# Optimization experiments

Hardware: AMD Instinct MI355X
Metric: run time of the kernel (lower is better)

Reference implementation:

```python
import jax, jax.numpy as jnp
import numpy as np

K = 3
CHUNK = 1000  # query chunk size for KNN distance tiles
EPS = 1e-8
GRID = 256.0  # coordinate extent (coords / stride in the original)


def _knn3(queries, refs):
    """Brute-force KNN (K=3, squared L2) computed in chunks to bound memory.
    queries: [Q,3], refs: [M,3] -> (dist [Q,3], idx [Q,3] int32)."""
    ref_sq = jnp.sum(refs * refs, axis=-1)  # [M]

    def chunk_fn(q):  # q: [CHUNK,3]
        d = jnp.sum(q * q, -1)[:, None] - 2.0 * (q @ refs.T) + ref_sq[None, :]
        d = jnp.maximum(d, 0.0)  # guard tiny negatives from cancellation
        neg_d, idx = jax.lax.top_k(-d, K)
        return -neg_d, idx

    Q = queries.shape[0]
    qs = queries.reshape(Q // CHUNK, CHUNK, 3)
    dists, idxs = jax.lax.map(chunk_fn, qs)
    return dists.reshape(Q, K), idxs.reshape(Q, K)


def setup_inputs() -> dict:
    key = jax.random.key(0)
    k1, k2, k3, k4 = jax.random.split(key, 4)
    N1, N2, C = 20000, 20000, 8
    xyz1 = jax.random.uniform(k1, (N1, 3), dtype=jnp.float32) * GRID
    point1 = jax.random.normal(k2, (N1, C), dtype=jnp.float32)
    xyz2 = jax.random.uniform(k3, (N2, 3), dtype=jnp.float32) * GRID
    motion = jax.random.normal(k4, (N2, C, 3), dtype=jnp.float32)
    return {"xyz1": xyz1, "point1": point1, "xyz2": xyz2, "motion": motion}


def reference(xyz1, point1, xyz2, motion):
    # Motion-compensated inter prediction tail of inter_prediction.forward:
    # per-channel warp, KNN(K=3) into frame 1, inverse-distance interpolation.
    N2, C, _ = motion.shape
    # xyz2_ = xyz2.unsqueeze(2) + motion -> [N2*C, 3]
    xyz2_ = (xyz2[:, None, :] + motion).reshape(N2 * C, 3)
    dist, idx = _knn3(xyz2_, xyz1)                 # [N2*C,3]
    dist = dist + EPS
    dist = dist.reshape(N2, C, K)
    idx = idx.reshape(N2, C, K)
    weights = 1.0 / dist
    weights = weights / jnp.maximum(weights.sum(axis=2, keepdims=True), 3.0)
    # knn_point1[n,c,k] = point1[idx[n,c,k], c]  (per-channel gather)
    pt = point1.T                                   # [C, N1]
    knn_point1 = pt[jnp.arange(C)[None, :, None], idx]  # [N2,C,3]
    predicted_point2 = (weights * knn_point1).sum(axis=2)  # [N2,C]
    return predicted_point2
```

## Files before the change

kernel.cpp:

```cpp
#include <hip/hip_runtime.h>
#include <math.h>

#define KNN_EPS 1e-8f
#define GH 16.0f
#define GC 16
#define NCELLS (GC * GC * GC)
#define MARGIN 1.0f
#define CAP 384
#define CAPR 64
#define CAPQ 192


__device__ __forceinline__ int cell_coord(float v) {
    int c = (int)floorf(v * (1.0f / GH));
    return min(max(c, 0), GC - 1);
}

__global__ void fused_scatter_kernel(
    const float* __restrict__ xyz1, int n1,
    const float* __restrict__ xyz2,
    const float* __restrict__ motion, int n2, int C,
    int* __restrict__ counts, int* __restrict__ qcounts,
    float4* __restrict__ rbuck, float4* __restrict__ qbuck,
    float4* __restrict__ refspill, int* __restrict__ rsn,
    float4* __restrict__ qspill, int* __restrict__ qsn)
{
#pragma clang fp contract(off)
    int i = blockIdx.x * blockDim.x + threadIdx.x;
    if (i < n1) {
        float x = xyz1[3 * i + 0];
        float y = xyz1[3 * i + 1];
        float z = xyz1[3 * i + 2];
        int cid = (cell_coord(z) * GC + cell_coord(y)) * GC + cell_coord(x);
        int pos = atomicAdd(&counts[cid], 1);
        float4 v = make_float4(x, y, z, __int_as_float(i));
        if (pos < CAPR) rbuck[cid * CAPR + pos] = v;
        else { int sp = atomicAdd(rsn, 1); refspill[sp] = v; }
    }
    int nq = n2 * C;
    if (i < nq) {
        int n = i / C;
        float qx = xyz2[3 * n + 0] + motion[3 * i + 0];
        float qy = xyz2[3 * n + 1] + motion[3 * i + 1];
        float qz = xyz2[3 * n + 2] + motion[3 * i + 2];
        int cid = (cell_coord(qz) * GC + cell_coord(qy)) * GC + cell_coord(qx);
        int pos = atomicAdd(&qcounts[cid], 1);
        float4 v = make_float4(qx, qy, qz, __int_as_float(i));
        if (pos < CAPQ) qbuck[cid * CAPQ + pos] = v;
        else { int sp = atomicAdd(qsn, 1); qspill[sp] = v; }
    }
}

__device__ __forceinline__ void top3_insert_lex(float d, int j,
                                                float& bd0, float& bd1, float& bd2,
                                                int& bi0, int& bi1, int& bi2) {
    if (d < bd2 || (d == bd2 && j < bi2)) {
        if (d < bd1 || (d == bd1 && j < bi1)) {
            bd2 = bd1; bi2 = bi1;
            if (d < bd0 || (d == bd0 && j < bi0)) {
                bd1 = bd0; bi1 = bi0;
                bd0 = d;   bi0 = j;
            } else {
                bd1 = d;   bi1 = j;
            }
        } else {
            bd2 = d;       bi2 = j;
        }
    }
}

__device__ __forceinline__ void eval_candidate(
    float4 r, float qx, float qy, float qz, float qsq,
    float& bd0, float& bd1, float& bd2, int& bi0, int& bi1, int& bi2) {
    int ridx = __float_as_int(r.w);
    float rsq = r.x * r.x + r.y * r.y;
    rsq = rsq + r.z * r.z;
    float t = fmaf(qz, r.z, fmaf(qy, r.y, qx * r.x));
    float h = qsq + rsq;
    float d = fmaxf(fmaf(-2.0f, t, h), 0.0f);
    top3_insert_lex(d, ridx, bd0, bd1, bd2, bi0, bi1, bi2);
}

__device__ __forceinline__ float cert_radius(float qx, float qy, float qz,
                                             int icx, int icy, int icz, int rho) {
    float R = INFINITY;
    if (icx - rho > 0)      R = fminf(R, qx - (float)(icx - rho) * GH);
    if (icx + rho < GC - 1) R = fminf(R, (float)(icx + rho + 1) * GH - qx);
    if (icy - rho > 0)      R = fminf(R, qy - (float)(icy - rho) * GH);
    if (icy + rho < GC - 1) R = fminf(R, (float)(icy + rho + 1) * GH - qy);
    if (icz - rho > 0)      R = fminf(R, qz - (float)(icz - rho) * GH);
    if (icz + rho < GC - 1) R = fminf(R, (float)(icz + rho + 1) * GH - qz);
    return R;
}

__device__ __forceinline__ void epilogue_store(
    float bd0, float bd1, float bd2, int bi0, int bi1, int bi2,
    int qid, int C, const float* __restrict__ point1, float* __restrict__ out) {
#pragma clang fp contract(off)
    float dd0 = bd0 + KNN_EPS;
    float dd1 = bd1 + KNN_EPS;
    float dd2 = bd2 + KNN_EPS;
    float w0 = 1.0f / dd0;
    float w1 = 1.0f / dd1;
    float w2 = 1.0f / dd2;
    float s  = w0 + w1;
    s = s + w2;
    float m = fmaxf(s, 3.0f);
    w0 = w0 / m;
    w1 = w1 / m;
    w2 = w2 / m;
    const int c = qid - (qid / C) * C;
    float p0 = point1[bi0 * C + c];
    float p1 = point1[bi1 * C + c];
    float p2 = point1[bi2 * C + c];
    float acc = w0 * p0 + w1 * p1;
    acc = acc + w2 * p2;
    out[qid] = acc;
}

__device__ void ring_search(float qx, float qy, float qz, float qsq,
                            const float4* __restrict__ rbuck,
                            const int* __restrict__ counts, int rspn,
                            const float4* __restrict__ refspill,
                            float& bd0, float& bd1, float& bd2,
                            int& bi0, int& bi1, int& bi2) {
    const int icx = cell_coord(qx);
    const int icy = cell_coord(qy);
    const int icz = cell_coord(qz);
    for (int k = 0; k < rspn; ++k)
        eval_candidate(refspill[k], qx, qy, qz, qsq, bd0, bd1, bd2, bi0, bi1, bi2);
    for (int rho = 0; rho < GC; ++rho) {
        for (int dz = -rho; dz <= rho; ++dz) {
            int cz = icz + dz;
            if (cz < 0 || cz >= GC) continue;
            int adz = (dz < 0) ? -dz : dz;
            for (int dy = -rho; dy <= rho; ++dy) {
                int cy = icy + dy;
                if (cy < 0 || cy >= GC) continue;
                int ady = (dy < 0) ? -dy : dy;
                int step = (adz == rho || ady == rho || rho == 0) ? 1 : 2 * rho;
                for (int dx = -rho; dx <= rho; dx += step) {
                    int cx = icx + dx;
                    if (cx < 0 || cx >= GC) continue;
                    int cid = (cz * GC + cy) * GC + cx;
                    int e = min(counts[cid], CAPR);
                    for (int s = 0; s < e; ++s)
                        eval_candidate(rbuck[cid * CAPR + s], qx, qy, qz, qsq,
                                       bd0, bd1, bd2, bi0, bi1, bi2);
                }
            }
        }
        float Rr = cert_radius(qx, qy, qz, icx, icy, icz, rho);
        if (bd2 + MARGIN <= Rr * Rr) break;
    }
}

__global__ __launch_bounds__(128, 8) void knn_cell_kernel(
    const float4* __restrict__ rbuck,
    const int*   __restrict__ counts,
    const float4* __restrict__ refspill,
    const int*   __restrict__ rsn,
    const float4* __restrict__ qbuck,
    const int*   __restrict__ qcounts,
    const float* __restrict__ point1,
    float* __restrict__ out,
    int C)
{
#pragma clang fp contract(off)
    const int cell = blockIdx.x;
    const int qn = min(qcounts[cell], CAPQ);
    if (qn == 0) return;
    const int qbase = cell * CAPQ;

    const int tid = threadIdx.x;
    const int lane = tid & 63;
    const int wave = tid >> 6;

    const int icx = cell & (GC - 1);
    const int icy = (cell >> 4) & (GC - 1);
    const int icz = cell >> 8;

    __shared__ float4 cand[CAP];
    __shared__ int rcid[27], rlen[27], rofs[27], rst[27];
    __shared__ int total_s, ovf_s, rsn_s;
    __shared__ float pbd[64][3];
    __shared__ int   pbi[64][3];

    if (tid < 27) {
        int dz = tid / 9 - 1, dy = (tid / 3) % 3 - 1, dx = tid % 3 - 1;
        int cz = icz + dz, cy = icy + dy, cx = icx + dx;
        int ok = (cz >= 0 && cz < GC && cy >= 0 && cy < GC && cx >= 0 && cx < GC);
        int cid = ok ? (cz * GC + cy) * GC + cx : 0;
        rcid[tid] = cid;
        rlen[tid] = ok ? min(counts[cid], CAPR) : 0;
    }
    if (tid == 32) rsn_s = *rsn;
    __syncthreads();
    if (tid == 0) {
        int run = 0, ovf = 0;
        for (int r = 0; r < 27; ++r) {
            int len = rlen[r];
            int st = min(len, CAP - run);
            rofs[r] = run; rst[r] = st;
            run += st;
            if (st < len) ovf = 1;
        }
        total_s = run; ovf_s = ovf;
    }
    __syncthreads();

    const int total = total_s;
    const int ovf = ovf_s;
    const int rspn = rsn_s;

    for (int i = tid; i < total; i += 128) {
        int lo = 0, hi = 26;
        while (lo < hi) {
            int mid = (lo + hi + 1) >> 1;
            if (rofs[mid] <= i) lo = mid; else hi = mid - 1;
        }
        cand[i] = rbuck[rcid[lo] * CAPR + (i - rofs[lo])];
    }
    __syncthreads();

    const int half = total >> 1;
    const int k0 = wave ? half : 0;
    const int k1 = wave ? total : half;

    const int niter = (qn + 63) >> 6;
    for (int it = 0; it < niter; ++it) {
        const int qo = it * 64 + lane;
        const bool active = qo < qn;
        float4 Q = qbuck[qbase + (active ? qo : 0)];
        const float qx = Q.x, qy = Q.y, qz = Q.z;
        const int qid = __float_as_int(Q.w);
        float qsq = qx * qx + qy * qy;
        qsq = qsq + qz * qz;

        float bd0 = INFINITY, bd1 = INFINITY, bd2 = INFINITY;
        int   bi0 = 0,        bi1 = 0,        bi2 = 0;

        int k = k0;
        for (; k + 4 <= k1; k += 4) {
            float4 c0 = cand[k + 0];
            float4 c1 = cand[k + 1];
            float4 c2 = cand[k + 2];
            float4 c3 = cand[k + 3];
            eval_candidate(c0, qx, qy, qz, qsq, bd0, bd1, bd2, bi0, bi1, bi2);
            eval_candidate(c1, qx, qy, qz, qsq, bd0, bd1, bd2, bi0, bi1, bi2);
            eval_candidate(c2, qx, qy, qz, qsq, bd0, bd1, bd2, bi0, bi1, bi2);
            eval_candidate(c3, qx, qy, qz, qsq, bd0, bd1, bd2, bi0, bi1, bi2);
        }
        for (; k < k1; ++k)
            eval_candidate(cand[k], qx, qy, qz, qsq, bd0, bd1, bd2, bi0, bi1, bi2);

        if (wave == 1) {
            pbd[lane][0] = bd0; pbd[lane][1] = bd1; pbd[lane][2] = bd2;
            pbi[lane][0] = bi0; pbi[lane][1] = bi1; pbi[lane][2] = bi2;
        }
        __syncthreads();

        if (wave == 0) {
            for (int m = 0; m < 3; ++m) {
                float d = pbd[lane][m];
                if (d < INFINITY)
                    top3_insert_lex(d, pbi[lane][m], bd0, bd1, bd2, bi0, bi1, bi2);
            }
            for (int k2 = 0; k2 < rspn; ++k2)
                eval_candidate(refspill[k2], qx, qy, qz, qsq,
                               bd0, bd1, bd2, bi0, bi1, bi2);
            if (ovf) {
                for (int r = 0; r < 27; ++r)
                    for (int kk = rst[r]; kk < rlen[r]; ++kk)
                        eval_candidate(rbuck[rcid[r] * CAPR + kk], qx, qy, qz, qsq,
                                       bd0, bd1, bd2, bi0, bi1, bi2);
            }
            float R = cert_radius(qx, qy, qz, icx, icy, icz, 1);
            if (!(bd2 + MARGIN <= R * R)) {
                for (int rho = 2; rho < GC; ++rho) {
                    for (int dz = -rho; dz <= rho; ++dz) {
                        int cz = icz + dz;
                        if (cz < 0 || cz >= GC) continue;
                        int adz = (dz < 0) ? -dz : dz;
                        for (int dy = -rho; dy <= rho; ++dy) {
                            int cy = icy + dy;
                            if (cy < 0 || cy >= GC) continue;
                            int ady = (dy < 0) ? -dy : dy;
                            int step = (adz == rho || ady == rho) ? 1 : 2 * rho;
                            for (int dx = -rho; dx <= rho; dx += step) {
                                int cx = icx + dx;
                                if (cx < 0 || cx >= GC) continue;
                                int cid = (cz * GC + cy) * GC + cx;
                                int e = min(counts[cid], CAPR);
                                for (int s = 0; s < e; ++s)
                                    eval_candidate(rbuck[cid * CAPR + s],
                                                   qx, qy, qz, qsq,
                                                   bd0, bd1, bd2, bi0, bi1, bi2);
                            }
                        }
                    }
                    float Rr = cert_radius(qx, qy, qz, icx, icy, icz, rho);
                    if (bd2 + MARGIN <= Rr * Rr) break;
                }
            }

            if (active)
                epilogue_store(bd0, bd1, bd2, bi0, bi1, bi2, qid, C, point1, out);
        }
        if (it + 1 < niter) __syncthreads();
    }
}

__global__ __launch_bounds__(256) void qspill_kernel(
    const float4* __restrict__ qspill, const int* __restrict__ qsn,
    const float4* __restrict__ rbuck, const int* __restrict__ counts,
    const float4* __restrict__ refspill, const int* __restrict__ rsn,
    const float* __restrict__ point1, float* __restrict__ out, int C)
{
#pragma clang fp contract(off)
    const int nsp = *qsn;
    const int rspn = *rsn;
    for (int s = blockIdx.x * blockDim.x + threadIdx.x; s < nsp;
         s += gridDim.x * blockDim.x) {
        float4 Q = qspill[s];
        const float qx = Q.x, qy = Q.y, qz = Q.z;
        const int qid = __float_as_int(Q.w);
        float qsq = qx * qx + qy * qy;
        qsq = qsq + qz * qz;
        float bd0 = INFINITY, bd1 = INFINITY, bd2 = INFINITY;
        int   bi0 = 0,        bi1 = 0,        bi2 = 0;
        ring_search(qx, qy, qz, qsq, rbuck, counts, rspn, refspill,
                    bd0, bd1, bd2, bi0, bi1, bi2);
        epilogue_store(bd0, bd1, bd2, bi0, bi1, bi2, qid, C, point1, out);
    }
}

extern "C" void kernel_launch(void* const* d_in, const int* in_sizes, int n_in,
                              void* d_out, int out_size, void* d_ws, size_t ws_size,
                              hipStream_t stream) {
    const float* xyz1   = (const float*)d_in[0];
    const float* point1 = (const float*)d_in[1];
    const float* xyz2   = (const float*)d_in[2];
    const float* motion = (const float*)d_in[3];
    float* out = (float*)d_out;

    const int n1 = in_sizes[0] / 3;
    const int n2 = in_sizes[2] / 3;
    const int C  = in_sizes[1] / n1;
    const int nq = n2 * C;

    char* ws = (char*)d_ws;
    size_t off = 0;
    auto alloc = [&](size_t bytes) {
        char* p = ws + off;
        off = (off + bytes + 255) & ~(size_t)255;
        return p;
    };
    float4* rbuck    = (float4*)alloc((size_t)NCELLS * CAPR * 16);
    float4* qbuck    = (float4*)alloc((size_t)NCELLS * CAPQ * 16);
    float4* refspill = (float4*)alloc((size_t)n1 * 16);
    float4* qspill   = (float4*)alloc((size_t)nq * 16);
    int*    zero     = (int*)alloc((size_t)(2 * NCELLS + 2) * 4);
    int* counts  = zero;
    int* qcounts = zero + NCELLS;
    int* rsn     = zero + 2 * NCELLS;
    int* qsn     = zero + 2 * NCELLS + 1;

    const int nmax = (n1 > nq) ? n1 : nq;

    hipMemsetAsync(zero, 0, (size_t)(2 * NCELLS + 2) * 4, stream);
    fused_scatter_kernel<<<(nmax + 255) / 256, 256, 0, stream>>>(
        xyz1, n1, xyz2, motion, n2, C,
        counts, qcounts, rbuck, qbuck, refspill, rsn, qspill, qsn);
    knn_cell_kernel<<<NCELLS, 128, 0, stream>>>(
        rbuck, counts, refspill, rsn, qbuck, qcounts, point1, out, C);
    qspill_kernel<<<4, 256, 0, stream>>>(
        qspill, qsn, rbuck, counts, refspill, rsn, point1, out, C);
}
```

Before: 169.4 us.

## Split candidate scan across four waves per cell block and parallelize prefix sum

Each cell block grows from two to four waves. Each wave scans a quarter of the staged candidate list, and wave 0 merges the partial top-3 lists from the other three waves through shared memory. The serial prefix over the 27 neighbour cells is replaced by a per-thread prefix computed by 27 threads. The goal is shorter per-block latency from more parallelism per query. In exchange, wave 0 does more merge work, and the larger blocks with launch bounds relaxed from 8 blocks per CU may lower occupancy or raise register pressure.

```diff
diff --git a/kernel.cpp b/kernel.cpp
--- a/kernel.cpp
+++ b/kernel.cpp
@@ -155,7 +155,7 @@
     }
 }
 
-__global__ __launch_bounds__(128, 8) void knn_cell_kernel(
+__global__ __launch_bounds__(256) void knn_cell_kernel(
     const float4* __restrict__ rbuck,
     const int*   __restrict__ counts,
     const float4* __restrict__ refspill,
@@ -183,8 +183,8 @@
     __shared__ float4 cand[CAP];
     __shared__ int rcid[27], rlen[27], rofs[27], rst[27];
     __shared__ int total_s, ovf_s, rsn_s;
-    __shared__ float pbd[64][3];
-    __shared__ int   pbi[64][3];
+    __shared__ float pbd[3][64][3];
+    __shared__ int   pbi[3][64][3];
 
     if (tid < 27) {
         int dz = tid / 9 - 1, dy = (tid / 3) % 3 - 1, dx = tid % 3 - 1;
@@ -196,16 +196,14 @@
     }
     if (tid == 32) rsn_s = *rsn;
     __syncthreads();
-    if (tid == 0) {
-        int run = 0, ovf = 0;
-        for (int r = 0; r < 27; ++r) {
-            int len = rlen[r];
-            int st = min(len, CAP - run);
-            rofs[r] = run; rst[r] = st;
-            run += st;
-            if (st < len) ovf = 1;
-        }
-        total_s = run; ovf_s = ovf;
+    if (tid < 27) {
+        int run = 0;
+        for (int r = 0; r < tid; ++r) run += rlen[r];
+        int len = rlen[tid];
+        int st = max(0, min(len, CAP - run));
+        rofs[tid] = min(run, CAP);
+        rst[tid] = st;
+        if (tid == 26) { total_s = min(run + len, CAP); ovf_s = (run + len > CAP); }
     }
     __syncthreads();
 
@@ -213,7 +211,7 @@
     const int ovf = ovf_s;
     const int rspn = rsn_s;
 
-    for (int i = tid; i < total; i += 128) {
+    for (int i = tid; i < total; i += 256) {
         int lo = 0, hi = 26;
         while (lo < hi) {
             int mid = (lo + hi + 1) >> 1;
@@ -223,9 +221,9 @@
     }
     __syncthreads();
 
-    const int half = total >> 1;
-    const int k0 = wave ? half : 0;
-    const int k1 = wave ? total : half;
+    const int qtr = total >> 2;
+    const int k0 = wave * qtr;
+    const int k1 = (wave == 3) ? total : k0 + qtr;
 
     const int niter = (qn + 63) >> 6;
     for (int it = 0; it < niter; ++it) {
@@ -254,18 +252,24 @@
         for (; k < k1; ++k)
             eval_candidate(cand[k], qx, qy, qz, qsq, bd0, bd1, bd2, bi0, bi1, bi2);
 
-        if (wave == 1) {
-            pbd[lane][0] = bd0; pbd[lane][1] = bd1; pbd[lane][2] = bd2;
-            pbi[lane][0] = bi0; pbi[lane][1] = bi1; pbi[lane][2] = bi2;
+        if (wave >= 1) {
+            pbd[wave - 1][lane][0] = bd0;
+            pbd[wave - 1][lane][1] = bd1;
+            pbd[wave - 1][lane][2] = bd2;
+            pbi[wave - 1][lane][0] = bi0;
+            pbi[wave - 1][lane][1] = bi1;
+            pbi[wave - 1][lane][2] = bi2;
         }
         __syncthreads();
 
         if (wave == 0) {
-            for (int m = 0; m < 3; ++m) {
-                float d = pbd[lane][m];
-                if (d < INFINITY)
-                    top3_insert_lex(d, pbi[lane][m], bd0, bd1, bd2, bi0, bi1, bi2);
-            }
+            for (int w = 0; w < 3; ++w)
+                for (int m = 0; m < 3; ++m) {
+                    float d = pbd[w][lane][m];
+                    if (d < INFINITY)
+                        top3_insert_lex(d, pbi[w][lane][m],
+                                        bd0, bd1, bd2, bi0, bi1, bi2);
+                }
             for (int k2 = 0; k2 < rspn; ++k2)
                 eval_candidate(refspill[k2], qx, qy, qz, qsq,
                                bd0, bd1, bd2, bi0, bi1, bi2);
@@ -372,7 +376,7 @@
     fused_scatter_kernel<<<(nmax + 255) / 256, 256, 0, stream>>>(
         xyz1, n1, xyz2, motion, n2, C,
         counts, qcounts, rbuck, qbuck, refspill, rsn, qspill, qsn);
-    knn_cell_kernel<<<NCELLS, 128, 0, stream>>>(
+    knn_cell_kernel<<<NCELLS, 256, 0, stream>>>(
         rbuck, counts, refspill, rsn, qbuck, qcounts, point1, out, C);
     qspill_kernel<<<4, 256, 0, stream>>>(
         qspill, qsn, rbuck, counts, refspill, rsn, point1, out, C);
```

New measurement: 191.2 us. 1.13x slower.

## Map one wave per cell and read neighbor buckets directly from global memory

Applied to the files above, without the earlier changes.

The per-cell KNN kernel now assigns one 64-lane wave to each grid cell, with four cells per 256-thread block. It drops the shared-memory candidate staging, the split of candidates across two waves, and the cross-wave merge with its barriers. Each lane scans the 27 neighbor buckets straight from global memory (cached) and then continues the ring search from radius 2 through a shared helper. This removes LDS staging and sync overhead but gives up shared-memory reuse and halves per-query parallelism, since one wave now evaluates every candidate.

```diff
diff --git a/kernel.cpp b/kernel.cpp
--- a/kernel.cpp
+++ b/kernel.cpp
@@ -6,7 +6,6 @@
 #define GC 16
 #define NCELLS (GC * GC * GC)
 #define MARGIN 1.0f
-#define CAP 384
 #define CAPR 64
 #define CAPQ 192
 
@@ -118,18 +117,20 @@
     out[qid] = acc;
 }
 
-__device__ void ring_search(float qx, float qy, float qz, float qsq,
-                            const float4* __restrict__ rbuck,
-                            const int* __restrict__ counts, int rspn,
-                            const float4* __restrict__ refspill,
-                            float& bd0, float& bd1, float& bd2,
-                            int& bi0, int& bi1, int& bi2) {
+__device__ void ring_search_from(float qx, float qy, float qz, float qsq,
+                                 int rho0,
+                                 const float4* __restrict__ rbuck,
+                                 const int* __restrict__ counts, int rspn,
+                                 const float4* __restrict__ refspill,
+                                 float& bd0, float& bd1, float& bd2,
+                                 int& bi0, int& bi1, int& bi2) {
     const int icx = cell_coord(qx);
     const int icy = cell_coord(qy);
     const int icz = cell_coord(qz);
-    for (int k = 0; k < rspn; ++k)
-        eval_candidate(refspill[k], qx, qy, qz, qsq, bd0, bd1, bd2, bi0, bi1, bi2);
-    for (int rho = 0; rho < GC; ++rho) {
+    if (rho0 == 0)
+        for (int k = 0; k < rspn; ++k)
+            eval_candidate(refspill[k], qx, qy, qz, qsq, bd0, bd1, bd2, bi0, bi1, bi2);
+    for (int rho = rho0; rho < GC; ++rho) {
         for (int dz = -rho; dz <= rho; ++dz) {
             int cz = icz + dz;
             if (cz < 0 || cz >= GC) continue;
@@ -155,7 +156,7 @@
     }
 }
 
-__global__ __launch_bounds__(128, 8) void knn_cell_kernel(
+__global__ __launch_bounds__(256) void knn_wave_kernel(
     const float4* __restrict__ rbuck,
     const int*   __restrict__ counts,
     const float4* __restrict__ refspill,
@@ -167,68 +168,20 @@
     int C)
 {
 #pragma clang fp contract(off)
-    const int cell = blockIdx.x;
+    const int wave = threadIdx.x >> 6;
+    const int lane = threadIdx.x & 63;
+    const int cell = blockIdx.x * 4 + wave;
+
     const int qn = min(qcounts[cell], CAPQ);
     if (qn == 0) return;
+    const int rspn = *rsn;
     const int qbase = cell * CAPQ;
-
-    const int tid = threadIdx.x;
-    const int lane = tid & 63;
-    const int wave = tid >> 6;
 
     const int icx = cell & (GC - 1);
     const int icy = (cell >> 4) & (GC - 1);
     const int icz = cell >> 8;
 
-    __shared__ float4 cand[CAP];
-    __shared__ int rcid[27], rlen[27], rofs[27], rst[27];
-    __shared__ int total_s, ovf_s, rsn_s;
-    __shared__ float pbd[64][3];
-    __shared__ int   pbi[64][3];
-
-    if (tid < 27) {
-        int dz = tid / 9 - 1, dy = (tid / 3) % 3 - 1, dx = tid % 3 - 1;
-        int cz = icz + dz, cy = icy + dy, cx = icx + dx;
-        int ok = (cz >= 0 && cz < GC && cy >= 0 && cy < GC && cx >= 0 && cx < GC);
-        int cid = ok ? (cz * GC + cy) * GC + cx : 0;
-        rcid[tid] = cid;
-        rlen[tid] = ok ? min(counts[cid], CAPR) : 0;
-    }
-    if (tid == 32) rsn_s = *rsn;
-    __syncthreads();
-    if (tid == 0) {
-        int run = 0, ovf = 0;
-        for (int r = 0; r < 27; ++r) {
-            int len = rlen[r];
-            int st = min(len, CAP - run);
-            rofs[r] = run; rst[r] = st;
-            run += st;
-            if (st < len) ovf = 1;
-        }
-        total_s = run; ovf_s = ovf;
-    }
-    __syncthreads();
-
-    const int total = total_s;
-    const int ovf = ovf_s;
-    const int rspn = rsn_s;
-
-    for (int i = tid; i < total; i += 128) {
-        int lo = 0, hi = 26;
-        while (lo < hi) {
-            int mid = (lo + hi + 1) >> 1;
-            if (rofs[mid] <= i) lo = mid; else hi = mid - 1;
-        }
-        cand[i] = rbuck[rcid[lo] * CAPR + (i - rofs[lo])];
-    }
-    __syncthreads();
-
-    const int half = total >> 1;
-    const int k0 = wave ? half : 0;
-    const int k1 = wave ? total : half;
-
-    const int niter = (qn + 63) >> 6;
-    for (int it = 0; it < niter; ++it) {
+    for (int it = 0; it * 64 < qn; ++it) {
         const int qo = it * 64 + lane;
         const bool active = qo < qn;
         float4 Q = qbuck[qbase + (active ? qo : 0)];
@@ -240,74 +193,48 @@
         float bd0 = INFINITY, bd1 = INFINITY, bd2 = INFINITY;
         int   bi0 = 0,        bi1 = 0,        bi2 = 0;
 
-        int k = k0;
-        for (; k + 4 <= k1; k += 4) {
-            float4 c0 = cand[k + 0];
-            float4 c1 = cand[k + 1];
-            float4 c2 = cand[k + 2];
-            float4 c3 = cand[k + 3];
-            eval_candidate(c0, qx, qy, qz, qsq, bd0, bd1, bd2, bi0, bi1, bi2);
-            eval_candidate(c1, qx, qy, qz, qsq, bd0, bd1, bd2, bi0, bi1, bi2);
-            eval_candidate(c2, qx, qy, qz, qsq, bd0, bd1, bd2, bi0, bi1, bi2);
-            eval_candidate(c3, qx, qy, qz, qsq, bd0, bd1, bd2, bi0, bi1, bi2);
-        }
-        for (; k < k1; ++k)
-            eval_candidate(cand[k], qx, qy, qz, qsq, bd0, bd1, bd2, bi0, bi1, bi2);
-
-        if (wave == 1) {
-            pbd[lane][0] = bd0; pbd[lane][1] = bd1; pbd[lane][2] = bd2;
-            pbi[lane][0] = bi0; pbi[lane][1] = bi1; pbi[lane][2] = bi2;
-        }
-        __syncthreads();
-
-        if (wave == 0) {
-            for (int m = 0; m < 3; ++m) {
-                float d = pbd[lane][m];
-                if (d < INFINITY)
-                    top3_insert_lex(d, pbi[lane][m], bd0, bd1, bd2, bi0, bi1, bi2);
-            }
-            for (int k2 = 0; k2 < rspn; ++k2)
-                eval_candidate(refspill[k2], qx, qy, qz, qsq,
-                               bd0, bd1, bd2, bi0, bi1, bi2);
-            if (ovf) {
-                for (int r = 0; r < 27; ++r)
-                    for (int kk = rst[r]; kk < rlen[r]; ++kk)
-                        eval_candidate(rbuck[rcid[r] * CAPR + kk], qx, qy, qz, qsq,
-                                       bd0, bd1, bd2, bi0, bi1, bi2);
-            }
-            float R = cert_radius(qx, qy, qz, icx, icy, icz, 1);
-            if (!(bd2 + MARGIN <= R * R)) {
-                for (int rho = 2; rho < GC; ++rho) {
-                    for (int dz = -rho; dz <= rho; ++dz) {
-                        int cz = icz + dz;
-                        if (cz < 0 || cz >= GC) continue;
-                        int adz = (dz < 0) ? -dz : dz;
-                        for (int dy = -rho; dy <= rho; ++dy) {
-                            int cy = icy + dy;
-                            if (cy < 0 || cy >= GC) continue;
-                            int ady = (dy < 0) ? -dy : dy;
-                            int step = (adz == rho || ady == rho) ? 1 : 2 * rho;
-                            for (int dx = -rho; dx <= rho; dx += step) {
-                                int cx = icx + dx;
-                                if (cx < 0 || cx >= GC) continue;
-                                int cid = (cz * GC + cy) * GC + cx;
-                                int e = min(counts[cid], CAPR);
-                                for (int s = 0; s < e; ++s)
-                                    eval_candidate(rbuck[cid * CAPR + s],
-                                                   qx, qy, qz, qsq,
-                                                   bd0, bd1, bd2, bi0, bi1, bi2);
-                            }
-                        }
+        for (int dz = -1; dz <= 1; ++dz) {
+            int cz = icz + dz;
+            if (cz < 0 || cz >= GC) continue;
+            for (int dy = -1; dy <= 1; ++dy) {
+                int cy = icy + dy;
+                if (cy < 0 || cy >= GC) continue;
+                int rowb = (cz * GC + cy) * GC;
+                for (int dx = -1; dx <= 1; ++dx) {
+                    int cx = icx + dx;
+                    if (cx < 0 || cx >= GC) continue;
+                    int cid = rowb + cx;
+                    int e = min(counts[cid], CAPR);
+                    const float4* p = rbuck + (size_t)cid * CAPR;
+                    int k = 0;
+                    for (; k + 4 <= e; k += 4) {
+                        float4 c0 = p[k + 0];
+                        float4 c1 = p[k + 1];
+                        float4 c2 = p[k + 2];
+                        float4 c3 = p[k + 3];
+                        eval_candidate(c0, qx, qy, qz, qsq, bd0, bd1, bd2, bi0, bi1, bi2);
+                        eval_candidate(c1, qx, qy, qz, qsq, bd0, bd1, bd2, bi0, bi1, bi2);
+                        eval_candidate(c2, qx, qy, qz, qsq, bd0, bd1, bd2, bi0, bi1, bi2);
+                        eval_candidate(c3, qx, qy, qz, qsq, bd0, bd1, bd2, bi0, bi1, bi2);
                     }
-                    float Rr = cert_radius(qx, qy, qz, icx, icy, icz, rho);
-                    if (bd2 + MARGIN <= Rr * Rr) break;
+                    for (; k < e; ++k)
+                        eval_candidate(p[k], qx, qy, qz, qsq, bd0, bd1, bd2, bi0, bi1, bi2);
                 }
             }
-
-            if (active)
-                epilogue_store(bd0, bd1, bd2, bi0, bi1, bi2, qid, C, point1, out);
         }
-        if (it + 1 < niter) __syncthreads();
+
+        for (int k2 = 0; k2 < rspn; ++k2)
+            eval_candidate(refspill[k2], qx, qy, qz, qsq,
+                           bd0, bd1, bd2, bi0, bi1, bi2);
+
+        float R = cert_radius(qx, qy, qz, icx, icy, icz, 1);
+        if (!(bd2 + MARGIN <= R * R)) {
+            ring_search_from(qx, qy, qz, qsq, 2, rbuck, counts, 0, refspill,
+                             bd0, bd1, bd2, bi0, bi1, bi2);
+        }
+
+        if (active)
+            epilogue_store(bd0, bd1, bd2, bi0, bi1, bi2, qid, C, point1, out);
     }
 }
 
@@ -329,8 +256,8 @@
         qsq = qsq + qz * qz;
         float bd0 = INFINITY, bd1 = INFINITY, bd2 = INFINITY;
         int   bi0 = 0,        bi1 = 0,        bi2 = 0;
-        ring_search(qx, qy, qz, qsq, rbuck, counts, rspn, refspill,
-                    bd0, bd1, bd2, bi0, bi1, bi2);
+        ring_search_from(qx, qy, qz, qsq, 0, rbuck, counts, rspn, refspill,
+                         bd0, bd1, bd2, bi0, bi1, bi2);
         epilogue_store(bd0, bd1, bd2, bi0, bi1, bi2, qid, C, point1, out);
     }
 }
@@ -372,7 +299,7 @@
     fused_scatter_kernel<<<(nmax + 255) / 256, 256, 0, stream>>>(
         xyz1, n1, xyz2, motion, n2, C,
         counts, qcounts, rbuck, qbuck, refspill, rsn, qspill, qsn);
-    knn_cell_kernel<<<NCELLS, 128, 0, stream>>>(
+    knn_wave_kernel<<<NCELLS / 4, 256, 0, stream>>>(
         rbuck, counts, refspill, rsn, qbuck, qcounts, point1, out, C);
     qspill_kernel<<<4, 256, 0, stream>>>(
         qspill, qsn, rbuck, counts, refspill, rsn, point1, out, C);
```

Result: slower. 201.7 us (+19.1%).
